# Performance work log

Measured on AMD Instinct MI355X. Metric: run time of the kernel, lower is better.

Reference implementation:

```python
import jax, jax.numpy as jnp
import numpy as np

NUM_GROUPS = 32
EPS = 1e-6


def group_norm(x, scale, bias):
    # x: [B, C, H, W]
    B, C, H, W = x.shape
    g = x.reshape(B, NUM_GROUPS, C // NUM_GROUPS, H, W)
    mean = g.mean(axis=(2, 3, 4), keepdims=True)
    var = g.var(axis=(2, 3, 4), keepdims=True)
    g = (g - mean) * jax.lax.rsqrt(var + EPS)
    x = g.reshape(B, C, H, W)
    return x * scale[None, :, None, None] + bias[None, :, None, None]


def nin(x, W, b):
    # 1x1 projection over channel dim: x [B,C,H,W], W [C,D], b [D]
    return jnp.einsum('bchw,cd->bdhw', x, W) + b[None, :, None, None]


def setup_inputs() -> dict:
    key = jax.random.key(0)
    ks = jax.random.split(key, 8)
    B, C, H, W = 32, 512, 32, 32
    # xavier_uniform bound for [C, C]
    bound = float(np.sqrt(6.0 / (C + C)))

    def xavier(k):
        return jax.random.uniform(k, (C, C), jnp.float32, -bound, bound)

    return {
        'x': jax.random.normal(ks[0], (B, C, H, W), jnp.float32),
        'gn_scale': jnp.ones((C,), jnp.float32),
        'gn_bias': jnp.zeros((C,), jnp.float32),
        'Wq': xavier(ks[1]), 'bq': jnp.zeros((C,), jnp.float32),
        'Wk': xavier(ks[2]), 'bk': jnp.zeros((C,), jnp.float32),
        'Wv': xavier(ks[3]), 'bv': jnp.zeros((C,), jnp.float32),
        'Wt': xavier(ks[4]), 'bt': jnp.zeros((C,), jnp.float32),
    }


def reference(x, gn_scale, gn_bias, Wq, bq, Wk, bk, Wv, bv, Wt, bt):
    B, C, H, W = x.shape
    h = group_norm(x, gn_scale, gn_bias)
    q = nin(h, Wq, bq)
    k = nin(h, Wk, bk)
    v = nin(h, Wv, bv)
    # full attention over H*W tokens
    w = jnp.einsum('bchw,bcij->bhwij', q, k) * (C ** -0.5)
    w = jax.nn.softmax(w.reshape(B, H, W, H * W), axis=-1).reshape(B, H, W, H, W)
    h = jnp.einsum('bhwij,bcij->bchw', w, v)
    h = nin(h, Wt, bt)
    return h + x
```

## Files before the change

### kernel.cpp

```cpp
#include <hip/hip_runtime.h>
#include <stdint.h>

#define Bsz 32
#define Cch 512
#define Ssp 1024
#define Grp 32
#define CPG 16

typedef unsigned short u16;
typedef __attribute__((ext_vector_type(8))) short bf16x8;
typedef __attribute__((ext_vector_type(4))) float f32x4;

__device__ __forceinline__ float bf2f(u16 u) {
  union { float f; uint32_t i; } w; w.i = ((uint32_t)u) << 16; return w.f;
}
__device__ __forceinline__ u16 f2bf(float f) {
  union { float f; uint32_t i; } w; w.f = f;
  uint32_t r = w.i + 0x7fffu + ((w.i >> 16) & 1u);
  return (u16)(r >> 16);
}

__device__ __forceinline__ void gload_lds16(const u16* g, u16* l) {
  __builtin_amdgcn_global_load_lds(
      (const __attribute__((address_space(1))) uint32_t*)g,
      (__attribute__((address_space(3))) uint32_t*)l, 16, 0, 0);
}

__global__ __launch_bounds__(256) void gnstats_kernel(
    const float* __restrict__ x, const float* __restrict__ scale,
    const float* __restrict__ bias, float2* __restrict__ stats) {
  int b = blockIdx.x >> 5;
  int g = blockIdx.x & 31;
  size_t base = ((size_t)b * Cch + (size_t)g * CPG) * Ssp;
  const float4* xv = (const float4*)(x + base);

  float sum = 0.f, sumsq = 0.f;
#pragma unroll
  for (int it = 0; it < 16; ++it) {
    float4 v = xv[threadIdx.x + 256 * it];
    sum += (v.x + v.y) + (v.z + v.w);
    sumsq += (v.x * v.x + v.y * v.y) + (v.z * v.z + v.w * v.w);
  }
#pragma unroll
  for (int off = 32; off > 0; off >>= 1) {
    sum += __shfl_xor(sum, off);
    sumsq += __shfl_xor(sumsq, off);
  }
  __shared__ float sm[8];
  int wid = threadIdx.x >> 6;
  if ((threadIdx.x & 63) == 0) { sm[wid] = sum; sm[4 + wid] = sumsq; }
  __syncthreads();
  sum = sm[0] + sm[1] + sm[2] + sm[3];
  sumsq = sm[4] + sm[5] + sm[6] + sm[7];
  float mean = sum * (1.f / 16384.f);
  float var = sumsq * (1.f / 16384.f) - mean * mean;
  float rstd = rsqrtf(var + 1e-6f);
  if (threadIdx.x < CPG) {
    int c = g * CPG + threadIdx.x;
    float sc = scale[c] * rstd;
    stats[(size_t)b * Cch + c] = make_float2(sc, bias[c] - mean * sc);
  }
}

__global__ __launch_bounds__(256) void xpose_gn(
    const float* __restrict__ x, const float2* __restrict__ stats,
    u16* __restrict__ xt) {
  __shared__ float T[64][65];
  int b = blockIdx.z;
  int s0 = blockIdx.x * 64, c0 = blockIdx.y * 64;
  int t = threadIdx.x;
  {
    int tx = t & 15, ty = t >> 4;
    const float* xb = x + ((size_t)b * Cch + c0) * Ssp + s0;
#pragma unroll
    for (int i = 0; i < 4; ++i) {
      int c = ty + 16 * i;
      float2 af = stats[(size_t)b * Cch + c0 + c];
      float4 v = *(const float4*)&xb[(size_t)c * Ssp + tx * 4];
      T[c][tx * 4 + 0] = v.x * af.x + af.y;
      T[c][tx * 4 + 1] = v.y * af.x + af.y;
      T[c][tx * 4 + 2] = v.z * af.x + af.y;
      T[c][tx * 4 + 3] = v.w * af.x + af.y;
    }
  }
  __syncthreads();
  {
    int cx = t & 7, sy = t >> 3;
    u16* ob = xt + ((size_t)b * Ssp + s0) * Cch + c0;
#pragma unroll
    for (int i = 0; i < 2; ++i) {
      int s = sy + 32 * i;
      union { u16 h[8]; uint4 v4; } pk;
#pragma unroll
      for (int j = 0; j < 8; ++j) pk.h[j] = f2bf(T[cx * 8 + j][s]);
      *(uint4*)&ob[(size_t)s * Cch + cx * 8] = pk.v4;
    }
  }
}

__global__ __launch_bounds__(256) void wxpose(
    const float* __restrict__ w0, const float* __restrict__ w1,
    const float* __restrict__ w2, const float* __restrict__ w3,
    u16* __restrict__ dst) {
  const float* W = blockIdx.z == 0 ? w0 : blockIdx.z == 1 ? w1
                   : blockIdx.z == 2 ? w2 : w3;
  u16* D = dst + (size_t)blockIdx.z * Cch * Cch;
  __shared__ float T[64][65];
  int d0 = blockIdx.x * 64, c0 = blockIdx.y * 64;
  int t = threadIdx.x;
  {
    int tx = t & 15, ty = t >> 4;
#pragma unroll
    for (int i = 0; i < 4; ++i) {
      int c = ty + 16 * i;
      float4 v = *(const float4*)&W[(size_t)(c0 + c) * Cch + d0 + tx * 4];
      T[c][tx * 4 + 0] = v.x; T[c][tx * 4 + 1] = v.y;
      T[c][tx * 4 + 2] = v.z; T[c][tx * 4 + 3] = v.w;
    }
  }
  __syncthreads();
  {
    int cx = t & 7, dy = t >> 3;
#pragma unroll
    for (int i = 0; i < 2; ++i) {
      int d = dy + 32 * i;
      union { u16 h[8]; uint4 v4; } pk;
#pragma unroll
      for (int j = 0; j < 8; ++j) pk.h[j] = f2bf(T[cx * 8 + j][d]);
      *(uint4*)&D[(size_t)(d0 + d) * Cch + c0 + cx * 8] = pk.v4;
    }
  }
}

template <int EPI>
__global__ __launch_bounds__(512, 2) void mfma_ntf(
    const u16* __restrict__ A, size_t sAb, int lda,
    const u16* __restrict__ B, size_t sBb, int ldb,
    void* __restrict__ Out, size_t sOb, int ldo,
    const float* __restrict__ bias,
    const float* __restrict__ bias2_or_resid, size_t sRb, int K) {
  __shared__ u16 As[2 * 16384];
  __shared__ u16 Bs[2 * 16384];

  const int nx = gridDim.x, ny = gridDim.y;
  const int pb = nx * ny;
  const int nwg = pb * gridDim.z;
  const int flat = (blockIdx.z * ny + blockIdx.y) * nx + blockIdx.x;
  const int qq = nwg >> 3, rr = nwg & 7;
  const int xcd = flat & 7, lid = flat >> 3;
  const int nf2 = (xcd < rr ? xcd * (qq + 1) : rr * (qq + 1) + (xcd - rr) * qq) + lid;
  const int b = nf2 / pb;
  const int rem = nf2 - b * pb;
  const int m0 = (rem / nx) * 256, n0 = (rem % nx) * 256;

  const int tid = threadIdx.x;
  const int lane = tid & 63, wave = tid >> 6;
  const int wm = wave >> 2, wn = wave & 3;
  const int quad = lane >> 4, l16 = lane & 15;

  const int sp = lane & 7, sq = lane >> 3;
  const int scl = sp ^ sq;
  const int srow = 2 * sq + (scl >> 2);
  const int scol = (scl & 3) * 8;

  const int vbase =
      ((l16 >> 1) << 6) + ((((l16 & 1) << 2) | quad) ^ (l16 >> 1)) * 8;

  const u16* Ab = A + (size_t)b * sAb + (size_t)m0 * lda;
  const u16* Bb = B + (size_t)b * sBb + (size_t)n0 * ldb;

  f32x4 acc[8][4] = {};

#define STGH(kh, kt1, nbuf)                                                    \
  {                                                                            \
    _Pragma("unroll") for (int i_ = 0; i_ < 2; ++i_) {                         \
      const int su_ = i_ * 8 + wave;                                           \
      gload_lds16(Ab + (size_t)(su_ * 16 + srow) * lda + (kt1) * 64 +          \
                      (kh) * 32 + scol,                                        \
                  As + (nbuf) * 16384 + (kh) * 8192 + su_ * 512);              \
      gload_lds16(Bb + (size_t)(su_ * 16 + srow) * ldb + (kt1) * 64 +          \
                      (kh) * 32 + scol,                                        \
                  Bs + (nbuf) * 16384 + (kh) * 8192 + su_ * 512);              \
    }                                                                          \
  }

#define LDA(mf, kk) \
  (*(const bf16x8*)&As[cur * 16384 + (kk) * 8192 + (wm * 8 + (mf)) * 512 + vbase])
#define LDB(nf, kk) \
  (*(const bf16x8*)&Bs[cur * 16384 + (kk) * 8192 + (wn * 4 + (nf)) * 512 + vbase])

#define BAR asm volatile("s_barrier" ::: "memory")
#define WAIT_VM(n) asm volatile("s_waitcnt vmcnt(" #n ")" ::: "memory")
#define WAIT_LGKM(n)                                      \
  asm volatile("s_waitcnt lgkmcnt(" #n ")" ::: "memory"); \
  __builtin_amdgcn_sched_barrier(0)
#define SB0 __builtin_amdgcn_sched_barrier(0)

  STGH(0, 0, 0)
  STGH(1, 0, 0)

  const int nk = K >> 6;
  bf16x8 bf[4], a[4], a2[4];
  for (int kt = 0; kt < nk; ++kt) {
    const int cur = kt & 1;
    const int nbuf = cur ^ 1;
    const bool nxt = (kt + 1 < nk);

    WAIT_VM(4);
    BAR;
#pragma unroll
    for (int i = 0; i < 4; ++i) bf[i] = LDB(i, 0);
#pragma unroll
    for (int i = 0; i < 4; ++i) a[i] = LDA(i, 0);
    SB0;
#pragma unroll
    for (int i = 0; i < 4; ++i) a2[i] = LDA(4 + i, 0);
    WAIT_LGKM(4);
    __builtin_amdgcn_s_setprio(1);
#pragma unroll
    for (int mf = 0; mf < 4; ++mf)
#pragma unroll
      for (int nf = 0; nf < 4; ++nf)
        acc[mf][nf] = __builtin_amdgcn_mfma_f32_16x16x32_bf16(
            a[mf], bf[nf], acc[mf][nf], 0, 0, 0);
    __builtin_amdgcn_s_setprio(0);
    if (nxt) STGH(0, kt + 1, nbuf)
    WAIT_LGKM(0);
    __builtin_amdgcn_s_setprio(1);
#pragma unroll
    for (int mf = 0; mf < 4; ++mf)
#pragma unroll
      for (int nf = 0; nf < 4; ++nf)
        acc[4 + mf][nf] = __builtin_amdgcn_mfma_f32_16x16x32_bf16(
            a2[mf], bf[nf], acc[4 + mf][nf], 0, 0, 0);
    __builtin_amdgcn_s_setprio(0);

    if (nxt) { WAIT_VM(4); } else { WAIT_VM(0); }
    BAR;
#pragma unroll
    for (int i = 0; i < 4; ++i) bf[i] = LDB(i, 1);
#pragma unroll
    for (int i = 0; i < 4; ++i) a[i] = LDA(i, 1);
    SB0;
#pragma unroll
    for (int i = 0; i < 4; ++i) a2[i] = LDA(4 + i, 1);
    WAIT_LGKM(4);
    __builtin_amdgcn_s_setprio(1);
#pragma unroll
    for (int mf = 0; mf < 4; ++mf)
#pragma unroll
      for (int nf = 0; nf < 4; ++nf)
        acc[mf][nf] = __builtin_amdgcn_mfma_f32_16x16x32_bf16(
            a[mf], bf[nf], acc[mf][nf], 0, 0, 0);
    __builtin_amdgcn_s_setprio(0);
    if (nxt) STGH(1, kt + 1, nbuf)
    WAIT_LGKM(0);
    __builtin_amdgcn_s_setprio(1);
#pragma unroll
    for (int mf = 0; mf < 4; ++mf)
#pragma unroll
      for (int nf = 0; nf < 4; ++nf)
        acc[4 + mf][nf] = __builtin_amdgcn_mfma_f32_16x16x32_bf16(
            a2[mf], bf[nf], acc[4 + mf][nf], 0, 0, 0);
    __builtin_amdgcn_s_setprio(0);
  }
#undef STGH
#undef LDA
#undef LDB

  const float SCALE = 0.044194173824159216f;
#pragma unroll
  for (int mf = 0; mf < 8; ++mf) {
#pragma unroll
    for (int nf = 0; nf < 4; ++nf) {
      int n = n0 + wn * 64 + nf * 16 + l16;
      float bn = 0.f;
      if constexpr (EPI == 0)
        bn = (n < 512) ? bias[n] : bias2_or_resid[n - 512];
#pragma unroll
      for (int reg = 0; reg < 4; ++reg) {
        int m = m0 + wm * 128 + mf * 16 + quad * 4 + reg;
        float v = acc[mf][nf][reg];
        size_t idx = (size_t)b * sOb + (size_t)m * ldo + n;
        if constexpr (EPI == 0) {
          ((u16*)Out)[idx] = f2bf(v + bn);
        } else if constexpr (EPI == 1) {
          ((u16*)Out)[idx] = f2bf(v + bias[m]);
        } else if constexpr (EPI == 2) {
          ((u16*)Out)[idx] = f2bf(v * SCALE);
        } else if constexpr (EPI == 3) {
          ((u16*)Out)[idx] = f2bf(v);
        } else {
          ((float*)Out)[idx] =
              v + bias[m] + bias2_or_resid[(size_t)b * sRb + (size_t)m * ldo + n];
        }
      }
    }
  }
}

__global__ __launch_bounds__(256) void softmax_kernel(u16* __restrict__ Sc) {
  size_t row = blockIdx.x;
  u16* rp = Sc + row * (size_t)Ssp;
  uint2 u = ((const uint2*)rp)[threadIdx.x];
  const u16* ph = (const u16*)&u;
  float v0 = bf2f(ph[0]), v1 = bf2f(ph[1]), v2 = bf2f(ph[2]), v3 = bf2f(ph[3]);
  float mx = fmaxf(fmaxf(v0, v1), fmaxf(v2, v3));
#pragma unroll
  for (int off = 32; off > 0; off >>= 1) mx = fmaxf(mx, __shfl_xor(mx, off));
  __shared__ float sm[4];
  __shared__ float sd[4];
  int wid = threadIdx.x >> 6;
  if ((threadIdx.x & 63) == 0) sm[wid] = mx;
  __syncthreads();
  mx = fmaxf(fmaxf(sm[0], sm[1]), fmaxf(sm[2], sm[3]));
  float e0 = __expf(v0 - mx), e1 = __expf(v1 - mx);
  float e2 = __expf(v2 - mx), e3 = __expf(v3 - mx);
  float s = e0 + e1 + e2 + e3;
#pragma unroll
  for (int off = 32; off > 0; off >>= 1) s += __shfl_xor(s, off);
  if ((threadIdx.x & 63) == 0) sd[wid] = s;
  __syncthreads();
  s = sd[0] + sd[1] + sd[2] + sd[3];
  float inv = 1.f / s;
  union { u16 s4[4]; uint2 v2; } pk;
  pk.s4[0] = f2bf(e0 * inv); pk.s4[1] = f2bf(e1 * inv);
  pk.s4[2] = f2bf(e2 * inv); pk.s4[3] = f2bf(e3 * inv);
  ((uint2*)rp)[threadIdx.x] = pk.v2;
}

extern "C" void kernel_launch(void* const* d_in, const int* in_sizes, int n_in,
                              void* d_out, int out_size, void* d_ws, size_t ws_size,
                              hipStream_t stream) {
  (void)in_sizes; (void)n_in; (void)out_size;
  const float* x   = (const float*)d_in[0];
  const float* gns = (const float*)d_in[1];
  const float* gnb = (const float*)d_in[2];
  const float* Wq  = (const float*)d_in[3];
  const float* bq  = (const float*)d_in[4];
  const float* Wk  = (const float*)d_in[5];
  const float* bk  = (const float*)d_in[6];
  const float* Wv  = (const float*)d_in[7];
  const float* bv  = (const float*)d_in[8];
  const float* Wt  = (const float*)d_in[9];
  const float* bt  = (const float*)d_in[10];
  float* out = (float*)d_out;
  char* ws = (char*)d_ws;

  const size_t QKSZ = (size_t)Bsz * Ssp * 1024 * 2;
  u16* qkt = (u16*)ws;
  u16* vv  = (u16*)(ws + QKSZ);
  u16* Wts = (u16*)(ws + (96ull << 20));
  float2* stats = (float2*)(ws + (98ull << 20));
  u16* xt  = (u16*)(ws + (99ull << 20));
  u16* Sc  = xt;
  u16* ot  = qkt;

  int NB;
  if (ws_size >= (163ull << 20)) NB = 32;
  else if (ws_size >= (131ull << 20)) NB = 16;
  else NB = 8;

  const size_t WSZ = (size_t)Cch * Cch;
  u16* Wvt = Wts + 2 * WSZ;
  u16* Wtt = Wts + 3 * WSZ;

  const size_t sSC  = (size_t)Ssp * Cch;
  const size_t sQK  = (size_t)Ssp * 1024;
  const size_t sCS  = (size_t)Cch * Ssp;
  const size_t sScB = (size_t)Ssp * Ssp;
  dim3 blk(256);
  dim3 blk8(512);

  gnstats_kernel<<<dim3(Bsz * Grp), blk, 0, stream>>>(x, gns, gnb, stats);
  xpose_gn<<<dim3(Ssp / 64, Cch / 64, Bsz), blk, 0, stream>>>(x, stats, xt);
  wxpose<<<dim3(8, 8, 4), blk, 0, stream>>>(Wq, Wk, Wv, Wt, Wts);

  mfma_ntf<0><<<dim3(4, 4, Bsz), blk8, 0, stream>>>(
      xt, sSC, Cch, Wts, 0, Cch, qkt, sQK, 1024, bq, bk, 0, Cch);
  mfma_ntf<1><<<dim3(4, 2, Bsz), blk8, 0, stream>>>(
      Wvt, 0, Cch, xt, sSC, Cch, vv, sCS, Ssp, bv, nullptr, 0, Cch);

  for (int b0 = 0; b0 < Bsz; b0 += NB) {
    int nb = (b0 + NB <= Bsz) ? NB : (Bsz - b0);
    mfma_ntf<2><<<dim3(4, 4, nb), blk8, 0, stream>>>(
        qkt + b0 * sQK, sQK, 1024, qkt + b0 * sQK + 512, sQK, 1024,
        Sc, sScB, Ssp, nullptr, nullptr, 0, Cch);
    softmax_kernel<<<dim3(nb * Ssp), blk, 0, stream>>>(Sc);
    mfma_ntf<3><<<dim3(2, 4, nb), blk8, 0, stream>>>(
        Sc, sScB, Ssp, vv + b0 * sCS, sCS, Ssp,
        ot + b0 * sSC, sSC, Cch, nullptr, nullptr, 0, Ssp);
  }

  mfma_ntf<4><<<dim3(4, 2, Bsz), blk8, 0, stream>>>(
      Wtt, 0, Cch, ot, sSC, Cch, out, sCS, Ssp, bt, x, sCS, Cch);
}
```

Measured before the change: 345.4 us.

## Fuse softmax into score GEMM epilogue and PV GEMM operand load

Removes the standalone softmax kernel. The QK^T GEMM epilogue now writes per-row partial max and sum-of-exp statistics for each 64-column slice. The PV GEMM first merges these 16 partials per row into a global max and inverse sum, then applies exp and normalization to the A fragments after they are read from LDS, just before the MFMAs. This saves a full read and write pass over the score matrix, at the cost of extra exp work inside the MFMA loop, because each score tile is re-exponentiated for every N tile. It also needs a shuffle reduction in the epilogue and a new stats buffer in the workspace.

```diff
diff --git a/kernel.cpp b/kernel.cpp
--- a/kernel.cpp
+++ b/kernel.cpp
@@ -24,6 +24,16 @@
   __builtin_amdgcn_global_load_lds(
       (const __attribute__((address_space(1))) uint32_t*)g,
       (__attribute__((address_space(3))) uint32_t*)l, 16, 0, 0);
+}
+
+__device__ __forceinline__ bf16x8 pxf(bf16x8 s, float M, float I) {
+  bf16x8 r;
+#pragma unroll
+  for (int j = 0; j < 8; ++j) {
+    float v = bf2f((u16)s[j]);
+    r[j] = (short)f2bf(__expf(v - M) * I);
+  }
+  return r;
 }
 
 __global__ __launch_bounds__(256) void gnstats_kernel(
@@ -141,6 +151,7 @@
     const float* __restrict__ bias2_or_resid, size_t sRb, int K) {
   __shared__ u16 As[2 * 16384];
   __shared__ u16 Bs[2 * 16384];
+  __shared__ float2 smrow[256];
 
   const int nx = gridDim.x, ny = gridDim.y;
   const int pb = nx * ny;
@@ -168,6 +179,31 @@
 
   const u16* Ab = A + (size_t)b * sAb + (size_t)m0 * lda;
   const u16* Bb = B + (size_t)b * sBb + (size_t)n0 * ldb;
+
+  float Mr[8], Ir[8];
+  if constexpr (EPI == 5) {
+    const float2* statsA = (const float2*)bias;
+    if (tid < 256) {
+      float2 pp[16];
+#pragma unroll
+      for (int j = 0; j < 16; ++j)
+        pp[j] = statsA[((size_t)b * 16 + j) * 1024 + m0 + tid];
+      float M = pp[0].x;
+#pragma unroll
+      for (int j = 1; j < 16; ++j) M = fmaxf(M, pp[j].x);
+      float S = 0.f;
+#pragma unroll
+      for (int j = 0; j < 16; ++j) S += __expf(pp[j].x - M) * pp[j].y;
+      smrow[tid] = make_float2(M, 1.f / S);
+    }
+    __syncthreads();
+#pragma unroll
+    for (int mf = 0; mf < 8; ++mf) {
+      float2 mi = smrow[wm * 128 + mf * 16 + l16];
+      Mr[mf] = mi.x;
+      Ir[mf] = mi.y;
+    }
+  }
 
   f32x4 acc[8][4] = {};
 
@@ -216,6 +252,10 @@
 #pragma unroll
     for (int i = 0; i < 4; ++i) a2[i] = LDA(4 + i, 0);
     WAIT_LGKM(4);
+    if constexpr (EPI == 5) {
+#pragma unroll
+      for (int i = 0; i < 4; ++i) a[i] = pxf(a[i], Mr[i], Ir[i]);
+    }
     __builtin_amdgcn_s_setprio(1);
 #pragma unroll
     for (int mf = 0; mf < 4; ++mf)
@@ -226,6 +266,10 @@
     __builtin_amdgcn_s_setprio(0);
     if (nxt) STGH(0, kt + 1, nbuf)
     WAIT_LGKM(0);
+    if constexpr (EPI == 5) {
+#pragma unroll
+      for (int i = 0; i < 4; ++i) a2[i] = pxf(a2[i], Mr[4 + i], Ir[4 + i]);
+    }
     __builtin_amdgcn_s_setprio(1);
 #pragma unroll
     for (int mf = 0; mf < 4; ++mf)
@@ -245,6 +289,10 @@
 #pragma unroll
     for (int i = 0; i < 4; ++i) a2[i] = LDA(4 + i, 1);
     WAIT_LGKM(4);
+    if constexpr (EPI == 5) {
+#pragma unroll
+      for (int i = 0; i < 4; ++i) a[i] = pxf(a[i], Mr[i], Ir[i]);
+    }
     __builtin_amdgcn_s_setprio(1);
 #pragma unroll
     for (int mf = 0; mf < 4; ++mf)
@@ -255,6 +303,10 @@
     __builtin_amdgcn_s_setprio(0);
     if (nxt) STGH(1, kt + 1, nbuf)
     WAIT_LGKM(0);
+    if constexpr (EPI == 5) {
+#pragma unroll
+      for (int i = 0; i < 4; ++i) a2[i] = pxf(a2[i], Mr[4 + i], Ir[4 + i]);
+    }
     __builtin_amdgcn_s_setprio(1);
 #pragma unroll
     for (int mf = 0; mf < 4; ++mf)
@@ -288,7 +340,7 @@
           ((u16*)Out)[idx] = f2bf(v + bias[m]);
         } else if constexpr (EPI == 2) {
           ((u16*)Out)[idx] = f2bf(v * SCALE);
-        } else if constexpr (EPI == 3) {
+        } else if constexpr (EPI == 5) {
           ((u16*)Out)[idx] = f2bf(v);
         } else {
           ((float*)Out)[idx] =
@@ -297,36 +349,34 @@
       }
     }
   }
-}
-
-__global__ __launch_bounds__(256) void softmax_kernel(u16* __restrict__ Sc) {
-  size_t row = blockIdx.x;
-  u16* rp = Sc + row * (size_t)Ssp;
-  uint2 u = ((const uint2*)rp)[threadIdx.x];
-  const u16* ph = (const u16*)&u;
-  float v0 = bf2f(ph[0]), v1 = bf2f(ph[1]), v2 = bf2f(ph[2]), v3 = bf2f(ph[3]);
-  float mx = fmaxf(fmaxf(v0, v1), fmaxf(v2, v3));
-#pragma unroll
-  for (int off = 32; off > 0; off >>= 1) mx = fmaxf(mx, __shfl_xor(mx, off));
-  __shared__ float sm[4];
-  __shared__ float sd[4];
-  int wid = threadIdx.x >> 6;
-  if ((threadIdx.x & 63) == 0) sm[wid] = mx;
-  __syncthreads();
-  mx = fmaxf(fmaxf(sm[0], sm[1]), fmaxf(sm[2], sm[3]));
-  float e0 = __expf(v0 - mx), e1 = __expf(v1 - mx);
-  float e2 = __expf(v2 - mx), e3 = __expf(v3 - mx);
-  float s = e0 + e1 + e2 + e3;
-#pragma unroll
-  for (int off = 32; off > 0; off >>= 1) s += __shfl_xor(s, off);
-  if ((threadIdx.x & 63) == 0) sd[wid] = s;
-  __syncthreads();
-  s = sd[0] + sd[1] + sd[2] + sd[3];
-  float inv = 1.f / s;
-  union { u16 s4[4]; uint2 v2; } pk;
-  pk.s4[0] = f2bf(e0 * inv); pk.s4[1] = f2bf(e1 * inv);
-  pk.s4[2] = f2bf(e2 * inv); pk.s4[3] = f2bf(e3 * inv);
-  ((uint2*)rp)[threadIdx.x] = pk.v2;
+
+  if constexpr (EPI == 2) {
+    float2* statsA = (float2*)bias;
+    const int slice = ((n0 >> 8) << 2) + wn;
+#pragma unroll
+    for (int mf = 0; mf < 8; ++mf) {
+#pragma unroll
+      for (int reg = 0; reg < 4; ++reg) {
+        float lm = -1e30f;
+#pragma unroll
+        for (int nf = 0; nf < 4; ++nf)
+          lm = fmaxf(lm, bf2f(f2bf(acc[mf][nf][reg] * SCALE)));
+#pragma unroll
+        for (int off = 8; off > 0; off >>= 1)
+          lm = fmaxf(lm, __shfl_xor(lm, off));
+        float ls = 0.f;
+#pragma unroll
+        for (int nf = 0; nf < 4; ++nf)
+          ls += __expf(bf2f(f2bf(acc[mf][nf][reg] * SCALE)) - lm);
+#pragma unroll
+        for (int off = 8; off > 0; off >>= 1) ls += __shfl_xor(ls, off);
+        if (l16 == 0) {
+          int row = m0 + wm * 128 + mf * 16 + quad * 4 + reg;
+          statsA[((size_t)b * 16 + slice) * 1024 + row] = make_float2(lm, ls);
+        }
+      }
+    }
+  }
 }
 
 extern "C" void kernel_launch(void* const* d_in, const int* in_sizes, int n_in,
@@ -357,9 +407,14 @@
   u16* ot  = qkt;
 
   int NB;
-  if (ws_size >= (163ull << 20)) NB = 32;
-  else if (ws_size >= (131ull << 20)) NB = 16;
-  else NB = 8;
+  float2* statsA;
+  if (ws_size >= (167ull << 20)) {
+    NB = 32; statsA = (float2*)(ws + (163ull << 20));
+  } else if (ws_size >= (134ull << 20)) {
+    NB = 16; statsA = (float2*)(ws + (131ull << 20));
+  } else {
+    NB = 8; statsA = (float2*)(ws + (98ull << 20));
+  }
 
   const size_t WSZ = (size_t)Cch * Cch;
   u16* Wvt = Wts + 2 * WSZ;
@@ -385,11 +440,10 @@
     int nb = (b0 + NB <= Bsz) ? NB : (Bsz - b0);
     mfma_ntf<2><<<dim3(4, 4, nb), blk8, 0, stream>>>(
         qkt + b0 * sQK, sQK, 1024, qkt + b0 * sQK + 512, sQK, 1024,
-        Sc, sScB, Ssp, nullptr, nullptr, 0, Cch);
-    softmax_kernel<<<dim3(nb * Ssp), blk, 0, stream>>>(Sc);
-    mfma_ntf<3><<<dim3(2, 4, nb), blk8, 0, stream>>>(
+        Sc, sScB, Ssp, (const float*)statsA, nullptr, 0, Cch);
+    mfma_ntf<5><<<dim3(2, 4, nb), blk8, 0, stream>>>(
         Sc, sScB, Ssp, vv + b0 * sCS, sCS, Ssp,
-        ot + b0 * sSC, sSC, Cch, nullptr, nullptr, 0, Ssp);
+        ot + b0 * sSC, sSC, Cch, (const float*)statsA, nullptr, 0, Ssp);
   }
 
   mfma_ntf<4><<<dim3(4, 2, Bsz), blk8, 0, stream>>>(
```

Result: slower. 400.1 us (+15.8%).
